# Optimization experiments

Measured on AMD Instinct MI355X. Metric: run time of the kernel, lower is better.

The kernel has to match this reference:

```python
import jax, jax.numpy as jnp
import numpy as np

DT = 1.0  # module init dt

def setup_inputs() -> dict:
    key = jax.random.key(0)
    k1, k2 = jax.random.split(key)
    x = jax.random.normal(k1, (8, 4096, 512), dtype=jnp.float32)
    w = jax.random.normal(k2, (512,), dtype=jnp.float32)
    return {"x": x, "w": w}

def reference(x, w):
    # h_t = h_{t-1} + dt*(x_t - relu(w)*h_{t-1}) = a*h_{t-1} + dt*x_t,  a = 1 - dt*relu(w)
    a = (1.0 - DT * jax.nn.relu(w)).astype(x.dtype)  # [d]
    h0 = jnp.zeros((x.shape[0], x.shape[2]), dtype=x.dtype)  # [b, d]
    xt = jnp.swapaxes(x, 0, 1)  # [t, b, d]

    def step(h, x_t):
        h_next = a * h + DT * x_t
        return h_next, h_next

    _, hs = jax.lax.scan(step, h0, xt)  # [t, b, d]
    return jnp.swapaxes(hs, 0, 1)  # [b, t, d] (return_sequences=True)
```

## Files before the change

kernel.cpp:

```cpp
#include <hip/hip_runtime.h>


#define RB 8
#define RT 4096
#define RD 512
#define RC 128
#define RL 32
#define LOG2_RL 5
#define DG (RD / 4)
#define PF 8

#define HB 1e15f

typedef float f32x4 __attribute__((ext_vector_type(4)));

__device__ __forceinline__ float sclamp(float v) {
    return fminf(fmaxf(v, -HB), HB);
}

__device__ __forceinline__ f32x4 ld4(const float4* __restrict__ p) {
    return *(const f32x4* __restrict__)p;
}

__global__ void __launch_bounds__(DG)
k_carry(const float4* __restrict__ x4, const float4* __restrict__ w4,
        float4* __restrict__ Lc) {
    const int g  = threadIdx.x;
    const int bc = blockIdx.x;
    const int b  = bc >> 7;
    const int c  = bc & (RC - 1);

    const float4 wv = w4[g];
    const float ax = 1.0f - fmaxf(wv.x, 0.0f);
    const float ay = 1.0f - fmaxf(wv.y, 0.0f);
    const float az = 1.0f - fmaxf(wv.z, 0.0f);
    const float aw = 1.0f - fmaxf(wv.w, 0.0f);

    const float4* __restrict__ xp = x4 + ((size_t)b * RT + (size_t)c * RL) * DG + g;

    f32x4 v[PF];
#pragma unroll
    for (int k = 0; k < PF; ++k) v[k] = ld4(xp + (size_t)k * DG);

    float hx = 0.f, hy = 0.f, hz = 0.f, hw = 0.f;
#pragma unroll
    for (int base = 0; base < RL; base += PF) {
        f32x4 n[PF];
        if (base + PF < RL) {
#pragma unroll
            for (int k = 0; k < PF; ++k)
                n[k] = ld4(xp + (size_t)(base + PF + k) * DG);
        }
#pragma unroll
        for (int k = 0; k < PF; ++k) {
            hx = sclamp(ax * hx + v[k].x);
            hy = sclamp(ay * hy + v[k].y);
            hz = sclamp(az * hz + v[k].z);
            hw = sclamp(aw * hw + v[k].w);
        }
        if (base + PF < RL) {
#pragma unroll
            for (int k = 0; k < PF; ++k) v[k] = n[k];
        }
    }
    Lc[(size_t)bc * DG + g] = make_float4(hx, hy, hz, hw);
}

__global__ void __launch_bounds__(DG)
k_final(const float4* __restrict__ x4, const float4* __restrict__ w4,
        const float4* __restrict__ Lc, float4* __restrict__ out4) {
    const int g  = threadIdx.x;
    const int bc = blockIdx.x;
    const int b  = bc >> 7;
    const int c  = bc & (RC - 1);

    const float4 wv = w4[g];
    const float ax = 1.0f - fmaxf(wv.x, 0.0f);
    const float ay = 1.0f - fmaxf(wv.y, 0.0f);
    const float az = 1.0f - fmaxf(wv.z, 0.0f);
    const float aw = 1.0f - fmaxf(wv.w, 0.0f);

    float Ax = ax, Ay = ay, Az = az, Aw = aw;
#pragma unroll
    for (int i = 0; i < LOG2_RL; ++i) {
        Ax = sclamp(Ax * Ax); Ay = sclamp(Ay * Ay);
        Az = sclamp(Az * Az); Aw = sclamp(Aw * Aw);
    }

    const float4* __restrict__ lp = Lc + (size_t)b * RC * DG + g;
    float hx = 0.f, hy = 0.f, hz = 0.f, hw = 0.f;
#pragma unroll 4
    for (int j = 0; j < c; ++j) {
        const float4 L = lp[(size_t)j * DG];
        hx = sclamp(Ax * hx + L.x);
        hy = sclamp(Ay * hy + L.y);
        hz = sclamp(Az * hz + L.z);
        hw = sclamp(Aw * hw + L.w);
    }

    const float4* __restrict__ xp = x4   + ((size_t)b * RT + (size_t)c * RL) * DG + g;
    float4*       __restrict__ op = out4 + ((size_t)b * RT + (size_t)c * RL) * DG + g;

    f32x4 v[PF];
#pragma unroll
    for (int k = 0; k < PF; ++k) v[k] = ld4(xp + (size_t)k * DG);

#pragma unroll
    for (int base = 0; base < RL; base += PF) {
        f32x4 n[PF];
        if (base + PF < RL) {
#pragma unroll
            for (int k = 0; k < PF; ++k)
                n[k] = ld4(xp + (size_t)(base + PF + k) * DG);
        }
#pragma unroll
        for (int k = 0; k < PF; ++k) {
            hx = sclamp(ax * hx + v[k].x);
            hy = sclamp(ay * hy + v[k].y);
            hz = sclamp(az * hz + v[k].z);
            hw = sclamp(aw * hw + v[k].w);
            f32x4 o = {hx, hy, hz, hw};
            __builtin_nontemporal_store(o, (f32x4*)&op[(size_t)(base + k) * DG]);
        }
        if (base + PF < RL) {
#pragma unroll
            for (int k = 0; k < PF; ++k) v[k] = n[k];
        }
    }
}

__global__ void __launch_bounds__(256)
rnn_seq_sat(const float* __restrict__ x, const float* __restrict__ w,
            float* __restrict__ out) {
    const int idx = blockIdx.x * blockDim.x + threadIdx.x;
    if (idx >= RB * RD) return;
    const int b = idx >> 9;
    const int d = idx & (RD - 1);
    const float a = 1.0f - fmaxf(w[d], 0.0f);
    const float* xp = x + (size_t)b * RT * RD + d;
    float* op = out + (size_t)b * RT * RD + d;
    float h = 0.f;
#pragma unroll 4
    for (int t = 0; t < RT; ++t) {
        h = sclamp(a * h + xp[(size_t)t * RD]);
        op[(size_t)t * RD] = h;
    }
}

extern "C" void kernel_launch(void* const* d_in, const int* in_sizes, int n_in,
                              void* d_out, int out_size, void* d_ws, size_t ws_size,
                              hipStream_t stream) {
    const float* x = (const float*)d_in[0];
    const float* w = (const float*)d_in[1];
    float* out = (float*)d_out;

    const size_t need = (size_t)RB * RC * DG * sizeof(float4);
    if (ws_size >= need) {
        const float4* x4 = (const float4*)x;
        const float4* w4 = (const float4*)w;
        float4* Lc = (float4*)d_ws;
        k_carry<<<dim3(RB * RC), dim3(DG), 0, stream>>>(x4, w4, Lc);
        k_final<<<dim3(RB * RC), dim3(DG), 0, stream>>>(x4, w4, Lc, (float4*)out);
    } else {
        rnn_seq_sat<<<dim3((RB * RD) / 256), dim3(256), 0, stream>>>(x, w, out);
    }
}
```

Measured before the change: 124.2 us.

## Write local chunk scans directly to output and fix up with carry powers

The carry kernel now also writes each chunk's zero-initialised local scan into the output. The second kernel no longer rereads x. Instead it rereads the output and adds the decayed carry (a^k times h_prev) to each element, skipping chunk 0, and it unrolls the chunk-carry loop by 8 with batched loads. This shortens the serial dependency in the fix pass but raises total memory traffic, since the output is written twice and read once. Clamping makes the split not exactly equivalent when values saturate.

After: 141.3 us. 13.8% more time.

```diff
diff --git a/kernel.cpp b/kernel.cpp
--- a/kernel.cpp
+++ b/kernel.cpp
@@ -23,8 +23,8 @@
 }
 
 __global__ void __launch_bounds__(DG)
-k_carry(const float4* __restrict__ x4, const float4* __restrict__ w4,
-        float4* __restrict__ Lc) {
+k_local(const float4* __restrict__ x4, const float4* __restrict__ w4,
+        float4* __restrict__ Lc, float4* __restrict__ out4) {
     const int g  = threadIdx.x;
     const int bc = blockIdx.x;
     const int b  = bc >> 7;
@@ -36,7 +36,8 @@
     const float az = 1.0f - fmaxf(wv.z, 0.0f);
     const float aw = 1.0f - fmaxf(wv.w, 0.0f);
 
-    const float4* __restrict__ xp = x4 + ((size_t)b * RT + (size_t)c * RL) * DG + g;
+    const float4* __restrict__ xp = x4   + ((size_t)b * RT + (size_t)c * RL) * DG + g;
+    float4*       __restrict__ op = out4 + ((size_t)b * RT + (size_t)c * RL) * DG + g;
 
     f32x4 v[PF];
 #pragma unroll
@@ -57,6 +58,7 @@
             hy = sclamp(ay * hy + v[k].y);
             hz = sclamp(az * hz + v[k].z);
             hw = sclamp(aw * hw + v[k].w);
+            op[(size_t)(base + k) * DG] = make_float4(hx, hy, hz, hw);
         }
         if (base + PF < RL) {
 #pragma unroll
@@ -67,12 +69,14 @@
 }
 
 __global__ void __launch_bounds__(DG)
-k_final(const float4* __restrict__ x4, const float4* __restrict__ w4,
-        const float4* __restrict__ Lc, float4* __restrict__ out4) {
+k_fix(const float4* __restrict__ w4, const float4* __restrict__ Lc,
+      float4* __restrict__ out4) {
     const int g  = threadIdx.x;
     const int bc = blockIdx.x;
     const int b  = bc >> 7;
     const int c  = bc & (RC - 1);
+
+    if (c == 0) return;
 
     const float4 wv = w4[g];
     const float ax = 1.0f - fmaxf(wv.x, 0.0f);
@@ -89,38 +93,57 @@
 
     const float4* __restrict__ lp = Lc + (size_t)b * RC * DG + g;
     float hx = 0.f, hy = 0.f, hz = 0.f, hw = 0.f;
-#pragma unroll 4
-    for (int j = 0; j < c; ++j) {
-        const float4 L = lp[(size_t)j * DG];
-        hx = sclamp(Ax * hx + L.x);
-        hy = sclamp(Ay * hy + L.y);
-        hz = sclamp(Az * hz + L.z);
-        hw = sclamp(Aw * hw + L.w);
+    int j = 0;
+    for (; j + 8 <= c; j += 8) {
+        f32x4 L0 = ld4(lp + (size_t)(j + 0) * DG);
+        f32x4 L1 = ld4(lp + (size_t)(j + 1) * DG);
+        f32x4 L2 = ld4(lp + (size_t)(j + 2) * DG);
+        f32x4 L3 = ld4(lp + (size_t)(j + 3) * DG);
+        f32x4 L4 = ld4(lp + (size_t)(j + 4) * DG);
+        f32x4 L5 = ld4(lp + (size_t)(j + 5) * DG);
+        f32x4 L6 = ld4(lp + (size_t)(j + 6) * DG);
+        f32x4 L7 = ld4(lp + (size_t)(j + 7) * DG);
+#define STEP(L)                                          \
+        hx = sclamp(Ax * hx + (L).x);                    \
+        hy = sclamp(Ay * hy + (L).y);                    \
+        hz = sclamp(Az * hz + (L).z);                    \
+        hw = sclamp(Aw * hw + (L).w);
+        STEP(L0) STEP(L1) STEP(L2) STEP(L3)
+        STEP(L4) STEP(L5) STEP(L6) STEP(L7)
     }
+    for (; j < c; ++j) {
+        f32x4 L = ld4(lp + (size_t)j * DG);
+        STEP(L)
+    }
+#undef STEP
 
-    const float4* __restrict__ xp = x4   + ((size_t)b * RT + (size_t)c * RL) * DG + g;
-    float4*       __restrict__ op = out4 + ((size_t)b * RT + (size_t)c * RL) * DG + g;
+    float4* __restrict__ op = out4 + ((size_t)b * RT + (size_t)c * RL) * DG + g;
 
     f32x4 v[PF];
 #pragma unroll
-    for (int k = 0; k < PF; ++k) v[k] = ld4(xp + (size_t)k * DG);
+    for (int k = 0; k < PF; ++k) v[k] = ld4(op + (size_t)k * DG);
 
+    float px = ax, py = ay, pz = az, pw = aw;
 #pragma unroll
     for (int base = 0; base < RL; base += PF) {
         f32x4 n[PF];
         if (base + PF < RL) {
 #pragma unroll
             for (int k = 0; k < PF; ++k)
-                n[k] = ld4(xp + (size_t)(base + PF + k) * DG);
+                n[k] = ld4(op + (size_t)(base + PF + k) * DG);
         }
 #pragma unroll
         for (int k = 0; k < PF; ++k) {
-            hx = sclamp(ax * hx + v[k].x);
-            hy = sclamp(ay * hy + v[k].y);
-            hz = sclamp(az * hz + v[k].z);
-            hw = sclamp(aw * hw + v[k].w);
-            f32x4 o = {hx, hy, hz, hw};
+            f32x4 o;
+            o.x = sclamp(v[k].x + px * hx);
+            o.y = sclamp(v[k].y + py * hy);
+            o.z = sclamp(v[k].z + pz * hz);
+            o.w = sclamp(v[k].w + pw * hw);
             __builtin_nontemporal_store(o, (f32x4*)&op[(size_t)(base + k) * DG]);
+            px = sclamp(px * ax);
+            py = sclamp(py * ay);
+            pz = sclamp(pz * az);
+            pw = sclamp(pw * aw);
         }
         if (base + PF < RL) {
 #pragma unroll
@@ -159,8 +182,8 @@
         const float4* x4 = (const float4*)x;
         const float4* w4 = (const float4*)w;
         float4* Lc = (float4*)d_ws;
-        k_carry<<<dim3(RB * RC), dim3(DG), 0, stream>>>(x4, w4, Lc);
-        k_final<<<dim3(RB * RC), dim3(DG), 0, stream>>>(x4, w4, Lc, (float4*)out);
+        k_local<<<dim3(RB * RC), dim3(DG), 0, stream>>>(x4, w4, Lc, (float4*)out);
+        k_fix<<<dim3(RB * RC), dim3(DG), 0, stream>>>(w4, Lc, (float4*)out);
     } else {
         rnn_seq_sat<<<dim3((RB * RD) / 256), dim3(256), 0, stream>>>(x, w, out);
     }
```
